# Optimization experiments

Measured on AMD Instinct MI355X. Metric: run time of the kernel, lower is better.

The kernel has to match this reference:

```python
import jax, jax.numpy as jnp
import numpy as np

B, DM, NH, NL, NP = 4, 768, 12, 3, 4
HD = DM // NH
H_IMG, W_IMG = 896, 896
LEVELS = [(H_IMG // 8, W_IMG // 8), (H_IMG // 16, W_IMG // 16), (H_IMG // 32, W_IMG // 32)]
QH, QW = H_IMG // 14, W_IMG // 14
LQ = QH * QW            # 4096 query tokens (stride-14 ViT grid)
LIN = sum(h * w for h, w in LEVELS)  # 16464 multi-scale value tokens


def setup_inputs() -> dict:
    key = jax.random.key(0)
    ks = jax.random.split(key, 14)
    s = 0.02
    return {
        "query": jax.random.normal(ks[0], (B, LQ, DM), jnp.float32),
        "feat": jax.random.normal(ks[1], (B, LIN, DM), jnp.float32),
        "ln_q_g": jnp.ones((DM,), jnp.float32),
        "ln_q_b": jnp.zeros((DM,), jnp.float32),
        "ln_f_g": jnp.ones((DM,), jnp.float32),
        "ln_f_b": jnp.zeros((DM,), jnp.float32),
        "W_off": jax.random.normal(ks[2], (DM, NH * NL * NP * 2), jnp.float32) * s,
        "b_off": jax.random.normal(ks[3], (NH * NL * NP * 2,), jnp.float32) * s,
        "W_attn": jax.random.normal(ks[4], (DM, NH * NL * NP), jnp.float32) * s,
        "b_attn": jax.random.normal(ks[5], (NH * NL * NP,), jnp.float32) * s,
        "W_val": jax.random.normal(ks[6], (DM, DM), jnp.float32) * s,
        "b_val": jnp.zeros((DM,), jnp.float32),
        "W_out": jax.random.normal(ks[7], (DM, DM), jnp.float32) * s,
        "b_out": jnp.zeros((DM,), jnp.float32),
        "gamma": jax.random.normal(ks[8], (DM,), jnp.float32) * s,
    }


def _ln(x, g, b, eps=1e-6):
    m = x.mean(-1, keepdims=True)
    v = ((x - m) ** 2).mean(-1, keepdims=True)
    return (x - m) * jax.lax.rsqrt(v + eps) * g + b


def _ref_points():
    # get_reference_points for the stride-14 query grid; pixel-center coords normalized
    ry, rx = jnp.meshgrid(
        (jnp.arange(QH, dtype=jnp.float32) + 0.5) / QH,
        (jnp.arange(QW, dtype=jnp.float32) + 0.5) / QW,
        indexing="ij",
    )
    return jnp.stack([rx.reshape(-1), ry.reshape(-1)], -1)  # (LQ, 2) in (x, y)


def _sample_level(v, loc, h_, w_):
    # v: (B, h_, w_, NH, HD); loc: (B, LQ, NH, NP, 2) normalized [0,1]
    # torch grid_sample bilinear, align_corners=False, zero padding
    x = loc[..., 0] * w_ - 0.5
    y = loc[..., 1] * h_ - 0.5
    x0 = jnp.floor(x)
    y0 = jnp.floor(y)
    wx = (x - x0)[..., None]
    wy = (y - y0)[..., None]
    x0i = x0.astype(jnp.int32)
    y0i = y0.astype(jnp.int32)
    bi = jnp.arange(B)[:, None, None, None]
    hi = jnp.arange(NH)[None, None, :, None]

    def g(yi, xi):
        valid = ((xi >= 0) & (xi < w_) & (yi >= 0) & (yi < h_)).astype(v.dtype)
        got = v[bi, jnp.clip(yi, 0, h_ - 1), jnp.clip(xi, 0, w_ - 1), hi]  # (B,LQ,NH,NP,HD)
        return got * valid[..., None]

    v00 = g(y0i, x0i)
    v01 = g(y0i, x0i + 1)
    v10 = g(y0i + 1, x0i)
    v11 = g(y0i + 1, x0i + 1)
    return v00 * (1 - wx) * (1 - wy) + v01 * wx * (1 - wy) + v10 * (1 - wx) * wy + v11 * wx * wy


def _injector(query, feat, ln_q_g, ln_q_b, ln_f_g, ln_f_b, W_off, b_off, W_attn, b_attn,
              W_val, b_val, W_out, b_out, gamma):
    q = _ln(query, ln_q_g, ln_q_b)
    f = _ln(feat, ln_f_g, ln_f_b)
    value = (f @ W_val + b_val).reshape(B, LIN, NH, HD)
    off = (q @ W_off + b_off).reshape(B, LQ, NH, NL, NP, 2)
    aw = jax.nn.softmax((q @ W_attn + b_attn).reshape(B, LQ, NH, NL * NP), axis=-1)
    aw = aw.reshape(B, LQ, NH, NL, NP)
    ref = _ref_points()  # (LQ, 2)
    offset_norm = jnp.array([[w, h] for h, w in LEVELS], jnp.float32)  # (NL, 2) = (W_, H_)
    loc = ref[None, :, None, None, None, :] + off / offset_norm[None, None, None, :, None, :]
    outs = []
    start = 0
    for lvl, (h_, w_) in enumerate(LEVELS):
        v = value[:, start:start + h_ * w_].reshape(B, h_, w_, NH, HD)
        outs.append(_sample_level(v, loc[:, :, :, lvl], h_, w_))
        start += h_ * w_
    samp = jnp.stack(outs, axis=3)  # (B, LQ, NH, NL, NP, HD)
    attn_out = (samp * aw[..., None]).sum(axis=(3, 4)).reshape(B, LQ, DM)
    attn_out = attn_out @ W_out + b_out
    return query + gamma * attn_out


def reference(query, feat, ln_q_g, ln_q_b, ln_f_g, ln_f_b, W_off, b_off, W_attn, b_attn,
              W_val, b_val, W_out, b_out, gamma):
    return _injector(query, feat, ln_q_g, ln_q_b, ln_f_g, ln_f_b, W_off, b_off, W_attn,
                     b_attn, W_val, b_val, W_out, b_out, gamma)
```

## Files before the change

kernel.cpp:

```cpp
#include <hip/hip_runtime.h>
#include <hip/hip_bf16.h>

typedef __hip_bfloat16 bf16;

#define BB    4
#define LQ    4096
#define LIN   16464
#define DM    768
#define NH    12
#define HD    64
#define K_DIM 768

typedef __attribute__((ext_vector_type(8))) __bf16 bfrag;
typedef __attribute__((ext_vector_type(4))) float  ffrag;

__device__ __forceinline__ void g2l16(const void* g, void* l) {
    __builtin_amdgcn_global_load_lds(
        (const __attribute__((address_space(1))) void*)g,
        (__attribute__((address_space(3))) void*)l, 16, 0, 0);
}

__device__ __forceinline__ int xcd_swz(int orig, int nwg) {
    int xcd = orig & 7, within = orig >> 3;
    int q = nwg >> 3, r = nwg & 7;
    return (xcd < r ? xcd * (q + 1) : r * (q + 1) + (xcd - r) * q) + within;
}

__global__ __launch_bounds__(256) void ln_kernel(
    const float* __restrict__ x, const float* __restrict__ g,
    const float* __restrict__ beta, bf16* __restrict__ y)
{
    int r = blockIdx.x * 4 + (threadIdx.x >> 6);
    int lane = threadIdx.x & 63;
    const float4* xr = (const float4*)(x + (size_t)r * DM);
    float4 v[3];
    #pragma unroll
    for (int i = 0; i < 3; i++) v[i] = xr[lane + 64 * i];
    float s = 0.f, ss = 0.f;
    #pragma unroll
    for (int i = 0; i < 3; i++) {
        s  += v[i].x + v[i].y + v[i].z + v[i].w;
        ss += v[i].x * v[i].x + v[i].y * v[i].y + v[i].z * v[i].z + v[i].w * v[i].w;
    }
    #pragma unroll
    for (int m = 1; m <= 32; m <<= 1) {
        s  += __shfl_xor(s, m);
        ss += __shfl_xor(ss, m);
    }
    float mean = s * (1.f / DM);
    float inv  = rsqrtf(ss * (1.f / DM) - mean * mean + 1e-6f);
    bf16* yr = y + (size_t)r * DM;
    #pragma unroll
    for (int i = 0; i < 3; i++) {
        float4 gg = ((const float4*)g)[lane + 64 * i];
        float4 bb = ((const float4*)beta)[lane + 64 * i];
        union { bf16 h[4]; uint2 u; } p;
        p.h[0] = __float2bfloat16((v[i].x - mean) * inv * gg.x + bb.x);
        p.h[1] = __float2bfloat16((v[i].y - mean) * inv * gg.y + bb.y);
        p.h[2] = __float2bfloat16((v[i].z - mean) * inv * gg.z + bb.z);
        p.h[3] = __float2bfloat16((v[i].w - mean) * inv * gg.w + bb.w);
        *(uint2*)(yr + (lane + 64 * i) * 4) = p.u;
    }
}

__global__ __launch_bounds__(256) void cast_transpose(
    const float* __restrict__ W, bf16* __restrict__ Wt, int N)
{
    __shared__ float t[32][33];
    int n0 = blockIdx.x * 32, k0 = blockIdx.y * 32;
    int tx = threadIdx.x & 31, ty = threadIdx.x >> 5;
    #pragma unroll
    for (int i = 0; i < 4; i++) {
        int k = k0 + ty + i * 8;
        int n = n0 + tx;
        t[ty + i * 8][tx] = (n < N) ? W[(size_t)k * N + n] : 0.f;
    }
    __syncthreads();
    #pragma unroll
    for (int i = 0; i < 4; i++) {
        int n = n0 + ty + i * 8;
        Wt[(size_t)n * K_DIM + k0 + tx] = __float2bfloat16(t[tx][ty + i * 8]);
    }
}

__global__ __launch_bounds__(512) void gemm256_value(
    const bf16*  __restrict__ A,
    const bf16*  __restrict__ Bt,
    const float* __restrict__ bias,
    bf16*        __restrict__ C,
    int M, int N)
{
    __shared__ __align__(16) char lds[131072];

    int tid  = threadIdx.x;
    int lane = tid & 63;
    int wave = tid >> 6;

    int nwg  = gridDim.x * gridDim.y;
    int orig = blockIdx.y * gridDim.x + blockIdx.x;
    int wg   = xcd_swz(orig, nwg);
    int bn = (wg % gridDim.x) * 256;
    int bm = (wg / gridDim.x) * 256;

    int ahalf = wave >> 2;
    int wc    = (wave & 3) * 64;
    int bhalf = (wave & 3) >> 1;
    int bcb   = (wave & 1) * 64;

    int ln15 = lane & 15, g = lane >> 4, l7 = lane & 7;

    ffrag acc[8][4] = {};

    int r_loc = tid >> 3;
    int koff  = (((tid & 7) ^ (r_loc & 7)) * 8);

    const bf16* gA[2][2];
    const bf16* gB[2][2];
    #pragma unroll
    for (int h = 0; h < 2; h++)
        #pragma unroll
        for (int ld = 0; ld < 2; ld++) {
            int ra = min(bm + h * 128 + ld * 64 + r_loc, M - 1);
            gA[h][ld] = A  + (size_t)ra * K_DIM + koff;
            int cb = bn + h * 128 + ld * 64 + r_loc;
            gB[h][ld] = Bt + (size_t)cb * K_DIM + koff;
        }

    auto stageA = [&](char* buf, int h, int kt) {
        g2l16(gA[h][0] + kt * 64, buf + h * 16384 + tid * 16);
        g2l16(gA[h][1] + kt * 64, buf + h * 16384 + 8192 + tid * 16);
    };
    auto stageB = [&](char* buf, int h, int kt) {
        g2l16(gB[h][0] + kt * 64, buf + 32768 + h * 16384 + tid * 16);
        g2l16(gB[h][1] + kt * 64, buf + 32768 + h * 16384 + 8192 + tid * 16);
    };

    stageA(lds, 0, 0); stageA(lds, 1, 0); stageB(lds, 0, 0); stageB(lds, 1, 0);

    int sby[2];
    sby[0] = ((0 * 4 + g) ^ l7) * 16;
    sby[1] = ((1 * 4 + g) ^ l7) * 16;

    #pragma unroll
    for (int kt = 0; kt < 12; kt++) {
        char* cur = lds + (kt & 1) * 65536;
        char* nxt = lds + ((kt & 1) ^ 1) * 65536;
        const char* Ac = cur + ahalf * 16384;
        const char* Bc = cur + 32768 + bhalf * 16384;

        if (kt + 1 < 12) {
            stageA(nxt, 0, kt + 1);
            asm volatile("s_waitcnt vmcnt(2)" ::: "memory");
        } else {
            asm volatile("s_waitcnt vmcnt(0)" ::: "memory");
        }
        __builtin_amdgcn_s_barrier();

        bfrag bf[4][2];
        #pragma unroll
        for (int nc = 0; nc < 4; nc++)
            #pragma unroll
            for (int ks = 0; ks < 2; ks++)
                bf[nc][ks] = *(const bfrag*)(Bc + (bcb + nc * 16 + ln15) * 128 + sby[ks]);
        {
            bfrag af[2][2];
            #pragma unroll
            for (int m2 = 0; m2 < 2; m2++)
                #pragma unroll
                for (int ks = 0; ks < 2; ks++)
                    af[m2][ks] = *(const bfrag*)(Ac + (m2 * 16 + ln15) * 128 + sby[ks]);
            __builtin_amdgcn_s_setprio(1);
            #pragma unroll
            for (int m2 = 0; m2 < 2; m2++)
                #pragma unroll
                for (int nc = 0; nc < 4; nc++)
                    #pragma unroll
                    for (int ks = 0; ks < 2; ks++)
                        acc[m2][nc] = __builtin_amdgcn_mfma_f32_16x16x32_bf16(
                            af[m2][ks], bf[nc][ks], acc[m2][nc], 0, 0, 0);
            __builtin_amdgcn_s_setprio(0);
        }
        __builtin_amdgcn_s_barrier();

        #pragma unroll
        for (int qd = 1; qd < 4; qd++) {
            if (kt + 1 < 12) {
                if (qd == 1) stageA(nxt, 1, kt + 1);
                else if (qd == 2) stageB(nxt, 0, kt + 1);
                else stageB(nxt, 1, kt + 1);
            }
            bfrag af[2][2];
            #pragma unroll
            for (int m2 = 0; m2 < 2; m2++)
                #pragma unroll
                for (int ks = 0; ks < 2; ks++)
                    af[m2][ks] = *(const bfrag*)(Ac + ((qd * 2 + m2) * 16 + ln15) * 128 + sby[ks]);
            __builtin_amdgcn_s_setprio(1);
            #pragma unroll
            for (int m2 = 0; m2 < 2; m2++)
                #pragma unroll
                for (int nc = 0; nc < 4; nc++)
                    #pragma unroll
                    for (int ks = 0; ks < 2; ks++)
                        acc[qd * 2 + m2][nc] = __builtin_amdgcn_mfma_f32_16x16x32_bf16(
                            af[m2][ks], bf[nc][ks], acc[qd * 2 + m2][nc], 0, 0, 0);
            __builtin_amdgcn_s_setprio(0);
            __builtin_amdgcn_s_barrier();
        }
    }

    int q4 = g * 4;
    #pragma unroll
    for (int mr = 0; mr < 8; mr++) {
        #pragma unroll
        for (int rr = 0; rr < 4; rr++) {
            int rg = bm + ahalf * 128 + mr * 16 + q4 + rr;
            if (rg < M) {
                #pragma unroll
                for (int nc = 0; nc < 4; nc++) {
                    int cg = bn + wc + nc * 16 + ln15;
                    C[(size_t)rg * N + cg] =
                        __float2bfloat16(acc[mr][nc][rr] + bias[cg]);
                }
            }
        }
    }
}

__device__ __forceinline__ void gemm128_body(
    const bf16*  __restrict__ A,
    const bf16*  __restrict__ Bt,
    const float* __restrict__ bias,
    void*        __restrict__ C,
    const float* __restrict__ resid,
    const float* __restrict__ gamma,
    const float* __restrict__ bias2,
    int M, int N, int mode, int nsplit, char* lds)
{
    int tid  = threadIdx.x;
    int lane = tid & 63;

    int nwg  = gridDim.x * gridDim.y;
    int orig = blockIdx.y * gridDim.x + blockIdx.x;
    int wg = xcd_swz(orig, nwg);
    int bn = (wg % gridDim.x) * 128;
    int bm = (wg / gridDim.x) * 128;

    int wave = tid >> 6;
    int wr = (wave & 1) * 64, wc = (wave >> 1) * 64;

    ffrag acc[4][4] = {};

    int rA = tid >> 2;
    int kb = (((tid & 3) ^ ((rA >> 1) & 3)) * 8);
    int ra0 = min(bm + rA, M - 1), ra1 = min(bm + 64 + rA, M - 1);
    const bf16* gA0 = A  + (size_t)ra0 * K_DIM + kb;
    const bf16* gA1 = A  + (size_t)ra1 * K_DIM + kb;
    const bf16* gB0 = Bt + (size_t)(bn + rA) * K_DIM + kb;
    const bf16* gB1 = Bt + (size_t)(bn + 64 + rA) * K_DIM + kb;

    int mrow = lane & 15;
    int kqs  = (((lane >> 4) ^ ((mrow >> 1) & 3)) * 8);

    auto stage = [&](char* buf, int kt) {
        const int ko = kt * 32;
        g2l16(gA0 + ko, buf + tid * 16);
        g2l16(gA1 + ko, buf + tid * 16 + 4096);
        g2l16(gB0 + ko, buf + 8192 + tid * 16);
        g2l16(gB1 + ko, buf + 8192 + tid * 16 + 4096);
    };

    stage(lds, 0);
    asm volatile("s_waitcnt vmcnt(0)" ::: "memory");
    __builtin_amdgcn_s_barrier();

    #pragma unroll
    for (int kt = 0; kt < 24; kt++) {
        char* cur = lds + (kt & 1) * 16384;
        char* nxt = lds + ((kt & 1) ^ 1) * 16384;
        if (kt + 1 < 24) stage(nxt, kt + 1);

        bfrag a[4], b[4];
        #pragma unroll
        for (int t = 0; t < 4; t++) {
            a[t] = *(const bfrag*)(cur + ((wr + t * 16 + mrow) * 32 + kqs) * 2);
            b[t] = *(const bfrag*)(cur + 8192 + ((wc + t * 16 + mrow) * 32 + kqs) * 2);
        }
        __builtin_amdgcn_s_setprio(1);
        #pragma unroll
        for (int i = 0; i < 4; i++)
            #pragma unroll
            for (int j = 0; j < 4; j++)
                acc[i][j] = __builtin_amdgcn_mfma_f32_16x16x32_bf16(
                    a[i], b[j], acc[i][j], 0, 0, 0);
        __builtin_amdgcn_s_setprio(0);

        asm volatile("s_waitcnt vmcnt(0)" ::: "memory");
        __builtin_amdgcn_s_barrier();
    }

    int q4 = (lane >> 4) * 4;
    #pragma unroll
    for (int i = 0; i < 4; i++) {
        #pragma unroll
        for (int rr = 0; rr < 4; rr++) {
            int rg = bm + wr + i * 16 + q4 + rr;
            if (rg < M) {
                #pragma unroll
                for (int j = 0; j < 4; j++) {
                    int cg = bn + wc + j * 16 + mrow;
                    if (cg < N) {
                        float bv = (mode == 3 && cg >= nsplit) ? bias2[cg - nsplit]
                                                               : bias[cg];
                        float v = acc[i][j][rr] + bv;
                        size_t idx = (size_t)rg * N + cg;
                        if (mode == 2)      ((float*)C)[idx] = resid[idx] + gamma[cg] * v;
                        else                ((float*)C)[idx] = v;
                    }
                }
            }
        }
    }
}

__global__ __launch_bounds__(256) void gemm128_comb(
    const bf16* __restrict__ A, const bf16* __restrict__ Bt,
    const float* __restrict__ bias, void* __restrict__ C,
    const float* __restrict__ bias2, int M, int N, int nsplit)
{
    __shared__ __align__(16) char lds[32768];
    gemm128_body(A, Bt, bias, C, nullptr, nullptr, bias2, M, N, 3, nsplit, lds);
}

__global__ __launch_bounds__(256) void gemm128_out(
    const bf16* __restrict__ A, const bf16* __restrict__ Bt,
    const float* __restrict__ bias, void* __restrict__ C,
    const float* __restrict__ resid, const float* __restrict__ gamma,
    int M, int N)
{
    __shared__ __align__(16) char lds[32768];
    gemm128_body(A, Bt, bias, C, resid, gamma, nullptr, M, N, 2, 0, lds);
}

__global__ __launch_bounds__(256) void sample_kernel(
    const bf16*  __restrict__ value,
    const float* __restrict__ comb,
    bf16*        __restrict__ attn)
{
    __shared__ float red[4][8][64];

    int wv   = threadIdx.x >> 6;
    int wg   = xcd_swz(blockIdx.x, gridDim.x);
    int unit = __builtin_amdgcn_readfirstlane((wg << 2) + wv);
    int lane = threadIdx.x & 63;
    int o   = lane & 7;
    int c8  = lane >> 3;
    int k   = c8 & 3;
    int dx  = k & 1, dy = k >> 1;
    int h  = unit % NH;
    int bq = unit / NH;
    int q  = bq & (LQ - 1);
    int b  = bq >> 12;

    const float* rowp = comb + (size_t)bq * 432;
    const float* ob = rowp + h * 24;
    const float* lg = rowp + 288 + h * 12;

    float4 lv0 = ((const float4*)lg)[0];
    float4 lv1 = ((const float4*)lg)[1];
    float4 lv2 = ((const float4*)lg)[2];
    float l[12] = {lv0.x, lv0.y, lv0.z, lv0.w,
                   lv1.x, lv1.y, lv1.z, lv1.w,
                   lv2.x, lv2.y, lv2.z, lv2.w};
    float mx = fmaxf(fmaxf(fmaxf(fmaxf(l[0], l[1]), fmaxf(l[2], l[3])),
                           fmaxf(fmaxf(l[4], l[5]), fmaxf(l[6], l[7]))),
                     fmaxf(fmaxf(l[8], l[9]), fmaxf(l[10], l[11])));
    float den = 0.f;
    #pragma unroll
    for (int i = 0; i < 12; i++) { l[i] = __expf(l[i] - mx); den += l[i]; }
    float rden = 1.f / den;

    float rx = ((q & 63) + 0.5f) * (1.f / 64.f);
    float ry = ((q >> 6) + 0.5f) * (1.f / 64.f);

    const bf16* vbase = value + (size_t)b * (LIN * NH * HD) + h * HD + o * 8;

    float acc[8] = {0.f};

    #pragma unroll
    for (int it = 0; it < 6; it++) {
        const int wl  = (it < 2) ? 112 : (it < 4 ? 56 : 28);
        const int slb = ((it < 2) ? 0 : (it < 4 ? 12544 : 15680)) * (NH * HD);
        int s = it * 2 + (c8 >> 2);
        float ox = ob[s * 2 + 0];
        float oy = ob[s * 2 + 1];
        float x = rx * wl + ox - 0.5f;
        float y = ry * wl + oy - 0.5f;
        float xf = floorf(x), yf = floorf(y);
        float wx = x - xf,  wy = y - yf;
        int xi = (int)xf + dx;
        int yi = (int)yf + dy;
        bool valid = ((unsigned)xi < (unsigned)wl) & ((unsigned)yi < (unsigned)wl);
        int xc = min(max(xi, 0), wl - 1);
        int yc = min(max(yi, 0), wl - 1);
        int idx = (yc * wl + xc) * (NH * HD) + slb;
        uint4 v = *(const uint4*)(vbase + idx);
        float aw = (c8 & 4) ? l[it * 2 + 1] : l[it * 2];
        float bw = (dx ? wx : 1.f - wx) * (dy ? wy : 1.f - wy);
        float w = valid ? aw * (bw * rden) : 0.f;
        const unsigned* u = (const unsigned*)&v;
        #pragma unroll
        for (int j = 0; j < 4; j++) {
            float f0 = __uint_as_float(u[j] << 16);
            float f1 = __uint_as_float(u[j] & 0xFFFF0000u);
            acc[j * 2 + 0] = fmaf(w, f0, acc[j * 2 + 0]);
            acc[j * 2 + 1] = fmaf(w, f1, acc[j * 2 + 1]);
        }
    }

    {
        float* rw = &red[wv][c8][0];
        int base = (o * 8 + c8 * 4) & 63;
        *(float4*)&rw[base] = float4{acc[0], acc[1], acc[2], acc[3]};
        *(float4*)&rw[(base + 4) & 63] = float4{acc[4], acc[5], acc[6], acc[7]};
    }
    asm volatile("s_waitcnt lgkmcnt(0)" ::: "memory");
    __builtin_amdgcn_sched_barrier(0);
    float sum = 0.f;
    #pragma unroll
    for (int s = 0; s < 8; s++)
        sum += red[wv][s][(lane + s * 4) & 63];

    attn[(size_t)bq * DM + h * HD + lane] = __float2bfloat16(sum);
}

extern "C" void kernel_launch(void* const* d_in, const int* in_sizes, int n_in,
                              void* d_out, int out_size, void* d_ws, size_t ws_size,
                              hipStream_t stream)
{
    const float* query  = (const float*)d_in[0];
    const float* feat   = (const float*)d_in[1];
    const float* ln_q_g = (const float*)d_in[2];
    const float* ln_q_b = (const float*)d_in[3];
    const float* ln_f_g = (const float*)d_in[4];
    const float* ln_f_b = (const float*)d_in[5];
    const float* W_off  = (const float*)d_in[6];
    const float* b_off  = (const float*)d_in[7];
    const float* W_attn = (const float*)d_in[8];
    const float* b_attn = (const float*)d_in[9];
    const float* W_val  = (const float*)d_in[10];
    const float* b_val  = (const float*)d_in[11];
    const float* W_out  = (const float*)d_in[12];
    const float* b_out  = (const float*)d_in[13];
    const float* gamma  = (const float*)d_in[14];
    float* out = (float*)d_out;

    char* ws = (char*)d_ws;
    char* od = (char*)d_out;
    const int M_F = BB * LIN;
    const int M_Q = BB * LQ;

    bf16*  value  = (bf16*)(ws);
    bf16*  f_ln   = (bf16*)(ws + 101154816);
    bf16*  Wt_out = (bf16*)(ws + 101154816);
    bf16*  q_ln   = (bf16*)(ws + 202309632);
    bf16*  attn   = (bf16*)(ws + 202309632);

    bf16*  Wt_val  = (bf16*)(od);
    bf16*  Wt_comb = (bf16*)(od + 1179648);
    float* comb    = (float*)(od + 2162688);

    cast_transpose<<<dim3(24, 24), 256, 0, stream>>>(W_val, Wt_val, 768);
    cast_transpose<<<dim3(9, 24), 256, 0, stream>>>(W_off, Wt_comb, 288);
    cast_transpose<<<dim3(7, 24), 256, 0, stream>>>(
        W_attn, Wt_comb + (size_t)288 * K_DIM, 144);

    ln_kernel<<<M_F / 4, 256, 0, stream>>>(feat, ln_f_g, ln_f_b, f_ln);
    ln_kernel<<<M_Q / 4, 256, 0, stream>>>(query, ln_q_g, ln_q_b, q_ln);

    gemm256_value<<<dim3(3, (M_F + 255) / 256), 512, 0, stream>>>(
        f_ln, Wt_val, b_val, value, M_F, DM);

    cast_transpose<<<dim3(24, 24), 256, 0, stream>>>(W_out, Wt_out, 768);

    gemm128_comb<<<dim3(4, M_Q / 128), 256, 0, stream>>>(
        q_ln, Wt_comb, b_off, comb, b_attn, M_Q, 432, 288);

    sample_kernel<<<(M_Q * NH) / 4, 256, 0, stream>>>(value, comb, attn);

    gemm128_out<<<dim3(6, M_Q / 128), 256, 0, stream>>>(
        attn, Wt_out, b_out, out, query, gamma, M_Q, DM);
}
```

Before: 707.7 us.

## Precompute sampling indices and bilinear weights in a separate prep kernel

Adds a prep kernel that runs once per (batch, query, head, point). It computes the softmax attention weights, the bilinear corner offsets and the validity-masked weights, and writes them as packed uint4 records to workspace. The sample kernel then just loads these records instead of redoing the softmax and coordinate maths in every lane. This removes redundant per-lane ALU work from the gather kernel, at the cost of an extra launch and about 25 MB of extra global write and read traffic.

```diff
diff --git a/kernel.cpp b/kernel.cpp
--- a/kernel.cpp
+++ b/kernel.cpp
@@ -342,9 +342,73 @@
     gemm128_body(A, Bt, bias, C, resid, gamma, nullptr, M, N, 2, 0, lds);
 }
 
+__global__ __launch_bounds__(256) void prep_kernel(
+    const float* __restrict__ comb, uint4* __restrict__ pre)
+{
+    int t  = blockIdx.x * 256 + threadIdx.x;
+    int p  = t % 12;
+    int uh = t / 12;
+    int h  = uh % NH;
+    int bq = uh / NH;
+    int q  = bq & (LQ - 1);
+    int b  = bq >> 12;
+
+    const float* rowp = comb + (size_t)bq * 432;
+    const float* lg = rowp + 288 + h * 12;
+
+    float4 a4 = ((const float4*)lg)[0];
+    float4 b4 = ((const float4*)lg)[1];
+    float4 c4 = ((const float4*)lg)[2];
+    float mx = fmaxf(fmaxf(fmaxf(fmaxf(a4.x, a4.y), fmaxf(a4.z, a4.w)),
+                           fmaxf(fmaxf(b4.x, b4.y), fmaxf(b4.z, b4.w))),
+                     fmaxf(fmaxf(c4.x, c4.y), fmaxf(c4.z, c4.w)));
+    float den = __expf(a4.x - mx) + __expf(a4.y - mx) + __expf(a4.z - mx) +
+                __expf(a4.w - mx) + __expf(b4.x - mx) + __expf(b4.y - mx) +
+                __expf(b4.z - mx) + __expf(b4.w - mx) + __expf(c4.x - mx) +
+                __expf(c4.y - mx) + __expf(c4.z - mx) + __expf(c4.w - mx);
+    float lp  = lg[p];
+    float awn = __expf(lp - mx) / den;
+
+    int lvl = p >> 2;
+    const int wl = (lvl == 0) ? 112 : (lvl == 1 ? 56 : 28);
+    const int sl = (lvl == 0) ? 0   : (lvl == 1 ? 12544 : 15680);
+
+    float2 oxy = *(const float2*)(rowp + h * 24 + p * 2);
+
+    float rx = ((q & 63) + 0.5f) * (1.f / 64.f);
+    float ry = ((q >> 6) + 0.5f) * (1.f / 64.f);
+    float x = rx * wl + oxy.x - 0.5f;
+    float y = ry * wl + oxy.y - 0.5f;
+    float xf = floorf(x), yf = floorf(y);
+    float wx = x - xf, wy = y - yf;
+    int x0 = (int)xf, x1 = x0 + 1;
+    int y0 = (int)yf, y1 = y0 + 1;
+    bool vx0 = (unsigned)x0 < (unsigned)wl, vx1 = (unsigned)x1 < (unsigned)wl;
+    bool vy0 = (unsigned)y0 < (unsigned)wl, vy1 = (unsigned)y1 < (unsigned)wl;
+    int x0c = min(max(x0, 0), wl - 1), x1c = min(max(x1, 0), wl - 1);
+    int y0c = min(max(y0, 0), wl - 1), y1c = min(max(y1, 0), wl - 1);
+
+    int base = b * LIN + sl;
+    int yb0 = (base + y0c * wl) * (NH * HD) + h * HD;
+    int yb1 = (base + y1c * wl) * (NH * HD) + h * HD;
+    int xb0 = x0c * (NH * HD);
+    int xb1 = x1c * (NH * HD);
+
+    float w0x = vx0 ? (1.f - wx) * awn : 0.f;
+    float w1x = vx1 ? wx * awn : 0.f;
+    float wy0f = vy0 ? (1.f - wy) : 0.f;
+    float wy1f = vy1 ? wy : 0.f;
+
+    uint4 i4 = {(unsigned)yb0, (unsigned)yb1, (unsigned)xb0, (unsigned)xb1};
+    uint4 w4 = {__float_as_uint(w0x), __float_as_uint(w1x),
+                __float_as_uint(wy0f), __float_as_uint(wy1f)};
+    pre[(size_t)t * 2 + 0] = i4;
+    pre[(size_t)t * 2 + 1] = w4;
+}
+
 __global__ __launch_bounds__(256) void sample_kernel(
     const bf16*  __restrict__ value,
-    const float* __restrict__ comb,
+    const uint4* __restrict__ pre,
     bf16*        __restrict__ attn)
 {
     __shared__ float red[4][8][64];
@@ -356,58 +420,25 @@
     int o   = lane & 7;
     int c8  = lane >> 3;
     int k   = c8 & 3;
-    int dx  = k & 1, dy = k >> 1;
+    bool dx = (k & 1) != 0, dy = (k >> 1) != 0;
+    bool hi = (c8 & 4) != 0;
     int h  = unit % NH;
     int bq = unit / NH;
-    int q  = bq & (LQ - 1);
-    int b  = bq >> 12;
-
-    const float* rowp = comb + (size_t)bq * 432;
-    const float* ob = rowp + h * 24;
-    const float* lg = rowp + 288 + h * 12;
-
-    float4 lv0 = ((const float4*)lg)[0];
-    float4 lv1 = ((const float4*)lg)[1];
-    float4 lv2 = ((const float4*)lg)[2];
-    float l[12] = {lv0.x, lv0.y, lv0.z, lv0.w,
-                   lv1.x, lv1.y, lv1.z, lv1.w,
-                   lv2.x, lv2.y, lv2.z, lv2.w};
-    float mx = fmaxf(fmaxf(fmaxf(fmaxf(l[0], l[1]), fmaxf(l[2], l[3])),
-                           fmaxf(fmaxf(l[4], l[5]), fmaxf(l[6], l[7]))),
-                     fmaxf(fmaxf(l[8], l[9]), fmaxf(l[10], l[11])));
-    float den = 0.f;
-    #pragma unroll
-    for (int i = 0; i < 12; i++) { l[i] = __expf(l[i] - mx); den += l[i]; }
-    float rden = 1.f / den;
-
-    float rx = ((q & 63) + 0.5f) * (1.f / 64.f);
-    float ry = ((q >> 6) + 0.5f) * (1.f / 64.f);
-
-    const bf16* vbase = value + (size_t)b * (LIN * NH * HD) + h * HD + o * 8;
+
+    const uint4* pp = pre + (size_t)unit * 24;
+    const bf16*  vbase = value + o * 8;
 
     float acc[8] = {0.f};
 
     #pragma unroll
     for (int it = 0; it < 6; it++) {
-        const int wl  = (it < 2) ? 112 : (it < 4 ? 56 : 28);
-        const int slb = ((it < 2) ? 0 : (it < 4 ? 12544 : 15680)) * (NH * HD);
-        int s = it * 2 + (c8 >> 2);
-        float ox = ob[s * 2 + 0];
-        float oy = ob[s * 2 + 1];
-        float x = rx * wl + ox - 0.5f;
-        float y = ry * wl + oy - 0.5f;
-        float xf = floorf(x), yf = floorf(y);
-        float wx = x - xf,  wy = y - yf;
-        int xi = (int)xf + dx;
-        int yi = (int)yf + dy;
-        bool valid = ((unsigned)xi < (unsigned)wl) & ((unsigned)yi < (unsigned)wl);
-        int xc = min(max(xi, 0), wl - 1);
-        int yc = min(max(yi, 0), wl - 1);
-        int idx = (yc * wl + xc) * (NH * HD) + slb;
+        const uint4* rec = pp + it * 4 + (hi ? 2 : 0);
+        uint4 i4 = rec[0];
+        uint4 w4 = rec[1];
+        int idx = (dy ? (int)i4.y : (int)i4.x) + (dx ? (int)i4.w : (int)i4.z);
+        float w = (dx ? __uint_as_float(w4.y) : __uint_as_float(w4.x)) *
+                  (dy ? __uint_as_float(w4.w) : __uint_as_float(w4.z));
         uint4 v = *(const uint4*)(vbase + idx);
-        float aw = (c8 & 4) ? l[it * 2 + 1] : l[it * 2];
-        float bw = (dx ? wx : 1.f - wx) * (dy ? wy : 1.f - wy);
-        float w = valid ? aw * (bw * rden) : 0.f;
         const unsigned* u = (const unsigned*)&v;
         #pragma unroll
         for (int j = 0; j < 4; j++) {
@@ -463,6 +494,7 @@
     bf16*  value  = (bf16*)(ws);
     bf16*  f_ln   = (bf16*)(ws + 101154816);
     bf16*  Wt_out = (bf16*)(ws + 101154816);
+    uint4* pre    = (uint4*)(ws + 101154816 + 4194304);
     bf16*  q_ln   = (bf16*)(ws + 202309632);
     bf16*  attn   = (bf16*)(ws + 202309632);
 
@@ -486,7 +518,9 @@
     gemm128_comb<<<dim3(4, M_Q / 128), 256, 0, stream>>>(
         q_ln, Wt_comb, b_off, comb, b_attn, M_Q, 432, 288);
 
-    sample_kernel<<<(M_Q * NH) / 4, 256, 0, stream>>>(value, comb, attn);
+    prep_kernel<<<(M_Q * NH * 12) / 256, 256, 0, stream>>>(comb, pre);
+
+    sample_kernel<<<(M_Q * NH) / 4, 256, 0, stream>>>(value, pre, attn);
 
     gemm128_out<<<dim3(6, M_Q / 128), 256, 0, stream>>>(
         attn, Wt_out, b_out, out, query, gamma, M_Q, DM);
```

Result: no change. 696.5 us (-1.6%).
